# Performance work log

Measured on AMD Instinct MI355X. Metric: run time of the kernel, lower is better.

Reference implementation:

```python
import jax, jax.numpy as jnp
import numpy as np

B, C, N, K = 8, 64, 4096, 16


def setup_inputs() -> dict:
    key = jax.random.key(0)
    k1, k2 = jax.random.split(key)
    x = jax.random.normal(k1, (B, C, N, 1), dtype=jnp.float32)
    edge_index = jax.random.randint(k2, (B, N, K), 0, N, dtype=jnp.int32)
    alpha = jnp.float32(1.0)  # AlphaLayer parameter, init 1.0
    return {"x": x, "edge_index": edge_index, "alpha": alpha}


def _aggregate_sum(x_nodes, edge_index):
    # x_nodes: [B, N, C]; edge_index: [B, N, K] neighbor ids per node.
    b, n, c = x_nodes.shape
    k = edge_index.shape[-1]
    idx = edge_index.reshape(b, n * k, 1).astype(jnp.int32)
    gathered = jnp.take_along_axis(x_nodes, idx, axis=1)  # [B, N*K, C]
    return gathered.reshape(b, n, k, c).sum(axis=2)       # [B, N, C]


def reference(x, edge_index, alpha):
    # x: [B, C, N, 1] -> permute(0,2,3,1) -> [B, N, 1, C]; W=1 so treat as [B, N, C]
    x_nodes = jnp.transpose(x[..., 0], (0, 2, 1))          # [B, N, C]
    m = _aggregate_sum(x_nodes, edge_index)                # [B, N, C]
    m = jnp.transpose(m, (0, 2, 1))[..., None]             # back to [B, C, N, 1]
    # AlphaLayer: x * (1 + alpha) + m
    return x * (1.0 + alpha) + m
```

## Files before the change

kernel.cpp:

```cpp
#include <hip/hip_runtime.h>

#define B_ 8
#define C_ 64
#define N_ 4096
#define K_ 16
#define THREADS 1024
#define NPT (N_ / THREADS)

__global__ __launch_bounds__(THREADS) void fused_k(const float* __restrict__ x,
                                                   const int* __restrict__ ei,
                                                   const float* __restrict__ alpha_p,
                                                   float* __restrict__ out) {
  __shared__ float2 xs[N_];
  const int bid = blockIdx.x;
  const int b   = bid & 7;
  const int c0  = (bid >> 3) * 2;
  const int t   = threadIdx.x;

  const float* xr0 = &x[((size_t)b * C_ + c0) * N_];
  const float* xr1 = xr0 + N_;

  float v0[NPT], v1[NPT];
#pragma unroll
  for (int i = 0; i < NPT; ++i) {
    const int n = t + i * THREADS;
    v0[i] = xr0[n];
    v1[i] = xr1[n];
    xs[n] = make_float2(v0[i], v1[i]);
  }
  __syncthreads();

  const float s = 1.0f + alpha_p[0];
  const int* eib = &ei[(size_t)b * N_ * K_];
  float* o0 = &out[((size_t)b * C_ + c0) * N_];
  float* o1 = o0 + N_;

#pragma unroll
  for (int i = 0; i < NPT; ++i) {
    const int n = t + i * THREADS;
    const int4* ep = reinterpret_cast<const int4*>(&eib[(size_t)n * K_]);
    int idx[K_];
    *reinterpret_cast<int4*>(&idx[0])  = ep[0];
    *reinterpret_cast<int4*>(&idx[4])  = ep[1];
    *reinterpret_cast<int4*>(&idx[8])  = ep[2];
    *reinterpret_cast<int4*>(&idx[12]) = ep[3];

    float ax = 0.f, ay = 0.f;
#pragma unroll
    for (int k = 0; k < K_; ++k) {
      const float2 g = xs[idx[k]];
      ax += g.x;
      ay += g.y;
    }
    o0[n] = v0[i] * s + ax;
    o1[n] = v1[i] * s + ay;
  }
}

extern "C" void kernel_launch(void* const* d_in, const int* in_sizes, int n_in,
                              void* d_out, int out_size, void* d_ws, size_t ws_size,
                              hipStream_t stream) {
  const float* x     = (const float*)d_in[0];
  const int*   ei    = (const int*)d_in[1];
  const float* alpha = (const float*)d_in[2];
  float*       out   = (float*)d_out;
  (void)d_ws; (void)ws_size;

  fused_k<<<B_ * (C_ / 2), THREADS, 0, stream>>>(x, ei, alpha, out);
}
```

Baseline: 11.88 us.

## Gather four channels per LDS read and split nodes across blocks

Each block now loads four channels into LDS as float4 and handles a quarter of the nodes, so every gathered neighbour read yields four channels. A XOR swizzle on the LDS slot is meant to reduce bank conflicts. Edge indices are loaded before the staging phase so their latency overlaps it. The cost is that each block stages the full 4096-node slab of x for only a quarter of the nodes, which raises redundant global reads of x 4x, and the 64KB of LDS per block limits occupancy.

```diff
diff --git a/kernel.cpp b/kernel.cpp
--- a/kernel.cpp
+++ b/kernel.cpp
@@ -4,56 +4,68 @@
 #define C_ 64
 #define N_ 4096
 #define K_ 16
-#define THREADS 1024
-#define NPT (N_ / THREADS)
+#define THREADS 512
+#define NQ 4
+#define NODES_PER_BLK (N_ / NQ)
+#define NPT (NODES_PER_BLK / THREADS)
+
+__device__ __forceinline__ int slot(int n) { return n ^ ((n >> 3) & 7); }
 
 __global__ __launch_bounds__(THREADS) void fused_k(const float* __restrict__ x,
                                                    const int* __restrict__ ei,
                                                    const float* __restrict__ alpha_p,
                                                    float* __restrict__ out) {
-  __shared__ float2 xs[N_];
+  __shared__ float4 xs[N_];
   const int bid = blockIdx.x;
   const int b   = bid & 7;
-  const int c0  = (bid >> 3) * 2;
+  const int cq  = (bid >> 3) & 15;
+  const int nq  = bid >> 7;
+  const int c0  = cq * 4;
+  const int n0  = nq * NODES_PER_BLK;
   const int t   = threadIdx.x;
 
-  const float* xr0 = &x[((size_t)b * C_ + c0) * N_];
-  const float* xr1 = xr0 + N_;
+  int idx[NPT][K_];
+  const int* eib = ei + ((size_t)b * N_ + n0) * K_;
+#pragma unroll
+  for (int q = 0; q < NPT; ++q) {
+    const int4* ep = reinterpret_cast<const int4*>(eib + (size_t)(t + q * THREADS) * K_);
+    *reinterpret_cast<int4*>(&idx[q][0])  = ep[0];
+    *reinterpret_cast<int4*>(&idx[q][4])  = ep[1];
+    *reinterpret_cast<int4*>(&idx[q][8])  = ep[2];
+    *reinterpret_cast<int4*>(&idx[q][12]) = ep[3];
+  }
 
-  float v0[NPT], v1[NPT];
+  const float* xb = x + ((size_t)b * C_ + c0) * N_;
 #pragma unroll
-  for (int i = 0; i < NPT; ++i) {
-    const int n = t + i * THREADS;
-    v0[i] = xr0[n];
-    v1[i] = xr1[n];
-    xs[n] = make_float2(v0[i], v1[i]);
+  for (int g = 0; g < N_ / (4 * THREADS); ++g) {
+    const int j = t + g * THREADS;
+    const float4 r0 = *reinterpret_cast<const float4*>(xb + 0 * N_ + 4 * j);
+    const float4 r1 = *reinterpret_cast<const float4*>(xb + 1 * N_ + 4 * j);
+    const float4 r2 = *reinterpret_cast<const float4*>(xb + 2 * N_ + 4 * j);
+    const float4 r3 = *reinterpret_cast<const float4*>(xb + 3 * N_ + 4 * j);
+    xs[slot(4 * j + 0)] = make_float4(r0.x, r1.x, r2.x, r3.x);
+    xs[slot(4 * j + 1)] = make_float4(r0.y, r1.y, r2.y, r3.y);
+    xs[slot(4 * j + 2)] = make_float4(r0.z, r1.z, r2.z, r3.z);
+    xs[slot(4 * j + 3)] = make_float4(r0.w, r1.w, r2.w, r3.w);
   }
   __syncthreads();
 
   const float s = 1.0f + alpha_p[0];
-  const int* eib = &ei[(size_t)b * N_ * K_];
-  float* o0 = &out[((size_t)b * C_ + c0) * N_];
-  float* o1 = o0 + N_;
-
 #pragma unroll
-  for (int i = 0; i < NPT; ++i) {
-    const int n = t + i * THREADS;
-    const int4* ep = reinterpret_cast<const int4*>(&eib[(size_t)n * K_]);
-    int idx[K_];
-    *reinterpret_cast<int4*>(&idx[0])  = ep[0];
-    *reinterpret_cast<int4*>(&idx[4])  = ep[1];
-    *reinterpret_cast<int4*>(&idx[8])  = ep[2];
-    *reinterpret_cast<int4*>(&idx[12]) = ep[3];
-
-    float ax = 0.f, ay = 0.f;
+  for (int q = 0; q < NPT; ++q) {
+    const int n = n0 + t + q * THREADS;
+    float4 acc = make_float4(0.f, 0.f, 0.f, 0.f);
 #pragma unroll
     for (int k = 0; k < K_; ++k) {
-      const float2 g = xs[idx[k]];
-      ax += g.x;
-      ay += g.y;
+      const float4 v = xs[slot(idx[q][k])];
+      acc.x += v.x; acc.y += v.y; acc.z += v.z; acc.w += v.w;
     }
-    o0[n] = v0[i] * s + ax;
-    o1[n] = v1[i] * s + ay;
+    const float4 sv = xs[slot(n)];
+    const size_t o = (size_t)(b * C_ + c0) * N_ + n;
+    out[o + 0 * N_] = sv.x * s + acc.x;
+    out[o + 1 * N_] = sv.y * s + acc.y;
+    out[o + 2 * N_] = sv.z * s + acc.z;
+    out[o + 3 * N_] = sv.w * s + acc.w;
   }
 }
 
@@ -66,5 +78,5 @@
   float*       out   = (float*)d_out;
   (void)d_ws; (void)ws_size;
 
-  fused_k<<<B_ * (C_ / 2), THREADS, 0, stream>>>(x, ei, alpha, out);
+  fused_k<<<B_ * (C_ / 4) * NQ, THREADS, 0, stream>>>(x, ei, alpha, out);
 }
```

After: 11.99 us. Within noise of the previous version (+0.9%).

## Pack eight channels as bf16 in LDS and split nodes across blocks

Applied to the files above, without the earlier changes.

Each block now stages eight channels per node as bf16 pairs packed into a uint4 in shared memory, and handles a quarter of the nodes with one node per thread. Neighbor gathers become one 16-byte LDS read covering eight channels, and edge indices are loaded once per eight channels instead of once per two. In exchange, the neighbor sum is computed from bf16-rounded values, which lowers accuracy, and the full node table is still staged redundantly by every block.

```diff
diff --git a/kernel.cpp b/kernel.cpp
--- a/kernel.cpp
+++ b/kernel.cpp
@@ -5,55 +5,72 @@
 #define N_ 4096
 #define K_ 16
 #define THREADS 1024
-#define NPT (N_ / THREADS)
+#define CG 8
+#define NQ 4
+
+__device__ __forceinline__ unsigned pack2(float lo, float hi) {
+  return ((__float_as_uint(lo) + 0x8000u) >> 16) |
+         ((__float_as_uint(hi) + 0x8000u) & 0xffff0000u);
+}
 
 __global__ __launch_bounds__(THREADS) void fused_k(const float* __restrict__ x,
                                                    const int* __restrict__ ei,
                                                    const float* __restrict__ alpha_p,
                                                    float* __restrict__ out) {
-  __shared__ float2 xs[N_];
+  __shared__ uint4 xs[N_];
   const int bid = blockIdx.x;
   const int b   = bid & 7;
-  const int c0  = (bid >> 3) * 2;
+  const int cg  = (bid >> 3) & 7;
+  const int nq  = bid >> 6;
+  const int c0  = cg * CG;
   const int t   = threadIdx.x;
 
-  const float* xr0 = &x[((size_t)b * C_ + c0) * N_];
-  const float* xr1 = xr0 + N_;
+  const float* xb = x + ((size_t)b * C_ + c0) * N_;
 
-  float v0[NPT], v1[NPT];
+  const int node = nq * (N_ / NQ) + t;
+  const int4* ep = reinterpret_cast<const int4*>(ei + ((size_t)b * N_ + node) * K_);
+  const int4 e0 = ep[0], e1 = ep[1], e2 = ep[2], e3 = ep[3];
+
 #pragma unroll
-  for (int i = 0; i < NPT; ++i) {
-    const int n = t + i * THREADS;
-    v0[i] = xr0[n];
-    v1[i] = xr1[n];
-    xs[n] = make_float2(v0[i], v1[i]);
+  for (int p = 0; p < N_ / THREADS; ++p) {
+    const int n = p * THREADS + t;
+    float r[CG];
+#pragma unroll
+    for (int c = 0; c < CG; ++c) r[c] = xb[c * N_ + n];
+    uint4 w;
+    w.x = pack2(r[0], r[1]);
+    w.y = pack2(r[2], r[3]);
+    w.z = pack2(r[4], r[5]);
+    w.w = pack2(r[6], r[7]);
+    xs[n] = w;
   }
   __syncthreads();
 
+  int idx[K_];
+  *reinterpret_cast<int4*>(&idx[0])  = e0;
+  *reinterpret_cast<int4*>(&idx[4])  = e1;
+  *reinterpret_cast<int4*>(&idx[8])  = e2;
+  *reinterpret_cast<int4*>(&idx[12]) = e3;
+
+  float acc[CG] = {0.f, 0.f, 0.f, 0.f, 0.f, 0.f, 0.f, 0.f};
+#pragma unroll
+  for (int k = 0; k < K_; ++k) {
+    const uint4 v = xs[idx[k]];
+    acc[0] += __uint_as_float(v.x << 16);
+    acc[1] += __uint_as_float(v.x & 0xffff0000u);
+    acc[2] += __uint_as_float(v.y << 16);
+    acc[3] += __uint_as_float(v.y & 0xffff0000u);
+    acc[4] += __uint_as_float(v.z << 16);
+    acc[5] += __uint_as_float(v.z & 0xffff0000u);
+    acc[6] += __uint_as_float(v.w << 16);
+    acc[7] += __uint_as_float(v.w & 0xffff0000u);
+  }
+
   const float s = 1.0f + alpha_p[0];
-  const int* eib = &ei[(size_t)b * N_ * K_];
-  float* o0 = &out[((size_t)b * C_ + c0) * N_];
-  float* o1 = o0 + N_;
-
+  float* ob = out + ((size_t)b * C_ + c0) * N_;
 #pragma unroll
-  for (int i = 0; i < NPT; ++i) {
-    const int n = t + i * THREADS;
-    const int4* ep = reinterpret_cast<const int4*>(&eib[(size_t)n * K_]);
-    int idx[K_];
-    *reinterpret_cast<int4*>(&idx[0])  = ep[0];
-    *reinterpret_cast<int4*>(&idx[4])  = ep[1];
-    *reinterpret_cast<int4*>(&idx[8])  = ep[2];
-    *reinterpret_cast<int4*>(&idx[12]) = ep[3];
-
-    float ax = 0.f, ay = 0.f;
-#pragma unroll
-    for (int k = 0; k < K_; ++k) {
-      const float2 g = xs[idx[k]];
-      ax += g.x;
-      ay += g.y;
-    }
-    o0[n] = v0[i] * s + ax;
-    o1[n] = v1[i] * s + ay;
+  for (int c = 0; c < CG; ++c) {
+    ob[c * N_ + node] = xb[c * N_ + node] * s + acc[c];
   }
 }
 
@@ -66,5 +83,5 @@
   float*       out   = (float*)d_out;
   (void)d_ws; (void)ws_size;
 
-  fused_k<<<B_ * (C_ / 2), THREADS, 0, stream>>>(x, ei, alpha, out);
+  fused_k<<<B_ * (C_ / CG) * NQ, THREADS, 0, stream>>>(x, ei, alpha, out);
 }
```

Result: faster. 11.59 us (-2.5%).
